# Kernel tuning notes

Hardware: AMD Instinct MI355X
Metric: run time of the kernel (lower is better)

The kernel has to match this reference:

```python
import jax, jax.numpy as jnp
import numpy as np

B, F, P = 16384, 4096, 32
D = F // P
EPS = 1e-5


def setup_inputs() -> dict:
    key = jax.random.key(0)
    ks = jax.random.split(key, 5)
    bound = 1.0 / np.sqrt(D)
    return {
        "x": jax.random.normal(ks[0], (B, F), dtype=jnp.float32),
        "weights1": jax.random.uniform(ks[1], (P, D, D), dtype=jnp.float32, minval=-bound, maxval=bound),
        "bias1": jax.random.uniform(ks[2], (F,), dtype=jnp.float32, minval=-bound, maxval=bound),
        "weights2": jax.random.uniform(ks[3], (P, D, D), dtype=jnp.float32, minval=-bound, maxval=bound),
        "bias2": jax.random.uniform(ks[4], (F,), dtype=jnp.float32, minval=-bound, maxval=bound),
        "gamma1": jnp.ones((F,), dtype=jnp.float32),
        "beta1": jnp.zeros((F,), dtype=jnp.float32),
        "gamma3": jnp.ones((F,), dtype=jnp.float32),
        "beta3": jnp.zeros((F,), dtype=jnp.float32),
    }


def _block_matmul(x, w):
    # x: [B, F] viewed as [B, P, D]; w: [P, D, D] block-diagonal blocks.
    # Equivalent to x @ block_diag(*w) without building the [F, F] matrix.
    xb = x.reshape(x.shape[0], P, D)
    return jnp.einsum("bpd,pde->bpe", xb, w).reshape(x.shape[0], F)


def _batchnorm(y, gamma, beta):
    # Training-mode BatchNorm1d: biased variance over the batch dim.
    mean = jnp.mean(y, axis=0)
    var = jnp.var(y, axis=0)
    return gamma * (y - mean) * jax.lax.rsqrt(var + EPS) + beta


def reference(x, weights1, bias1, weights2, bias2, gamma1, beta1, gamma3, beta3):
    o1 = jnp.tanh(_batchnorm(_block_matmul(x, weights1) + bias1, gamma1, beta1))
    o2 = _block_matmul(o1, weights2) + bias2
    o3 = jnp.tanh(_batchnorm(o2 + x, gamma3, beta3))
    return o3
```

## Files before the change

kernel.cpp:

```cpp
#include <hip/hip_runtime.h>
#include <cstdint>
#include <cstddef>

#define B_ 16384
#define F_ 4096
#define P_ 32
#define D_ 128
#define STRIPS 16
#define TILES 32

using f32x4 = __attribute__((ext_vector_type(4))) float;
using s16x8 = __attribute__((ext_vector_type(8))) short;

__device__ inline unsigned short bf16_rn(float f) {
    union { float f; uint32_t u; } v; v.f = f;
    uint32_t u = v.u;
    return (unsigned short)((u + 0x7FFFu + ((u >> 16) & 1u)) >> 16);
}
__device__ inline float bf16_to_f32(unsigned short h) {
    union { uint32_t u; float f; } v; v.u = ((uint32_t)h) << 16;
    return v.f;
}
__device__ inline float fast_tanh(float z) {
    float e = __expf(2.f * z);
    return 1.f - 2.f / (e + 1.f);
}

__device__ inline void stage_w(const float* __restrict__ Wp,
                               short* s_whi, short* s_wlo, int tid) {
    for (int it = 0; it < 32; ++it) {
        int idx = it * 256 + tid;
        int c  = idx & 127;
        int kp = idx >> 7;
        float w0 = Wp[(2 * kp) * D_ + c];
        float w1 = Wp[(2 * kp + 1) * D_ + c];
        unsigned short h0 = bf16_rn(w0), h1 = bf16_rn(w1);
        float l0 = w0 - bf16_to_f32(h0);
        float l1 = w1 - bf16_to_f32(h1);
        unsigned short g0 = bf16_rn(l0), g1 = bf16_rn(l1);
        uint32_t hi = (uint32_t)h0 | ((uint32_t)h1 << 16);
        uint32_t lo = (uint32_t)g0 | ((uint32_t)g1 << 16);
        int boff = c * 256 + ((4 * kp) ^ ((c & 7) << 4));
        *(uint32_t*)((char*)s_whi + boff) = hi;
        *(uint32_t*)((char*)s_wlo + boff) = lo;
    }
}

__device__ inline s16x8 read_b(const short* s_w, int col, int skbytes) {
    int boff = col * 256 + (skbytes ^ ((col & 7) << 4));
    return *(const s16x8*)((const char*)s_w + boff);
}

__global__ __launch_bounds__(256) void k_gemm1(
    const float* __restrict__ x, const float* __restrict__ W1,
    const float* __restrict__ bias1, float* __restrict__ y1,
    float* __restrict__ sum1, float* __restrict__ sumsq1)
{
    __shared__ short s_whi[D_ * D_];
    __shared__ short s_wlo[D_ * D_];
    const int tid = threadIdx.x;
    const int bid = blockIdx.x;
    const int p = bid / STRIPS;
    const int strip = bid % STRIPS;
    stage_w(W1 + (size_t)p * D_ * D_, s_whi, s_wlo, tid);
    __syncthreads();

    const int wave = tid >> 6, lane = tid & 63;
    const int l15 = lane & 15, l4 = lane >> 4;
    const int colbase = wave * 32;

    float bi[2]; int gcol[2];
#pragma unroll
    for (int j = 0; j < 2; ++j) {
        gcol[j] = p * D_ + colbase + j * 16 + l15;
        bi[j] = bias1[gcol[j]];
    }
    float csum[2] = {0.f, 0.f}, csq[2] = {0.f, 0.f};

    for (int it = 0; it < TILES; ++it) {
        const int m0 = strip * (TILES * 32) + it * 32;
        f32x4 av[2][4][2];
#pragma unroll
        for (int i = 0; i < 2; ++i)
#pragma unroll
            for (int s = 0; s < 4; ++s) {
                const float* ptr = x + (size_t)(m0 + i * 16 + l15) * F_
                                     + p * D_ + s * 32 + l4 * 8;
                av[i][s][0] = *(const f32x4*)ptr;
                av[i][s][1] = *(const f32x4*)(ptr + 4);
            }
        f32x4 zero = {0.f, 0.f, 0.f, 0.f};
        f32x4 acc[2][2];
#pragma unroll
        for (int i = 0; i < 2; ++i)
#pragma unroll
            for (int j = 0; j < 2; ++j) acc[i][j] = zero;

#pragma unroll
        for (int s = 0; s < 4; ++s) {
            s16x8 a[2];
#pragma unroll
            for (int i = 0; i < 2; ++i)
#pragma unroll
                for (int t = 0; t < 4; ++t) {
                    a[i][t]     = (short)bf16_rn(av[i][s][0][t]);
                    a[i][t + 4] = (short)bf16_rn(av[i][s][1][t]);
                }
            const int sk = s * 64 + l4 * 16;
#pragma unroll
            for (int j = 0; j < 2; ++j) {
                const int col = colbase + j * 16 + l15;
                s16x8 bh = read_b(s_whi, col, sk);
                s16x8 bl = read_b(s_wlo, col, sk);
#pragma unroll
                for (int i = 0; i < 2; ++i) {
                    acc[i][j] = __builtin_amdgcn_mfma_f32_16x16x32_bf16(a[i], bh, acc[i][j], 0, 0, 0);
                    acc[i][j] = __builtin_amdgcn_mfma_f32_16x16x32_bf16(a[i], bl, acc[i][j], 0, 0, 0);
                }
            }
        }
#pragma unroll
        for (int i = 0; i < 2; ++i)
#pragma unroll
            for (int j = 0; j < 2; ++j)
#pragma unroll
                for (int r = 0; r < 4; ++r) {
                    float v = acc[i][j][r] + bi[j];
                    int row = m0 + i * 16 + l4 * 4 + r;
                    y1[(size_t)row * F_ + gcol[j]] = v;
                    csum[j] += v;
                    csq[j]  += v * v;
                }
    }
#pragma unroll
    for (int j = 0; j < 2; ++j) {
        float s = csum[j], q = csq[j];
        s += __shfl_xor(s, 16); q += __shfl_xor(q, 16);
        s += __shfl_xor(s, 32); q += __shfl_xor(q, 32);
        if (l4 == 0) {
            atomicAdd(&sum1[gcol[j]], s);
            atomicAdd(&sumsq1[gcol[j]], q);
        }
    }
}

__global__ __launch_bounds__(256) void k_gemm2(
    const float* __restrict__ x, float* yb ,
    const float* __restrict__ W2, const float* __restrict__ bias2,
    const float* __restrict__ scale1, const float* __restrict__ shift1,
    float* __restrict__ sum3, float* __restrict__ sumsq3)
{
    __shared__ short s_whi[D_ * D_];
    __shared__ short s_wlo[D_ * D_];
    __shared__ float s_sc[D_];
    __shared__ float s_sh[D_];
    const int tid = threadIdx.x;
    const int bid = blockIdx.x;
    const int p = bid / STRIPS;
    const int strip = bid % STRIPS;
    stage_w(W2 + (size_t)p * D_ * D_, s_whi, s_wlo, tid);
    if (tid < D_) {
        s_sc[tid] = scale1[p * D_ + tid];
        s_sh[tid] = shift1[p * D_ + tid];
    }
    __syncthreads();

    const int wave = tid >> 6, lane = tid & 63;
    const int l15 = lane & 15, l4 = lane >> 4;
    const int colbase = wave * 32;

    float bi[2]; int gcol[2];
#pragma unroll
    for (int j = 0; j < 2; ++j) {
        gcol[j] = p * D_ + colbase + j * 16 + l15;
        bi[j] = bias2[gcol[j]];
    }
    float csum[2] = {0.f, 0.f}, csq[2] = {0.f, 0.f};

    for (int it = 0; it < TILES; ++it) {
        const int m0 = strip * (TILES * 32) + it * 32;
        f32x4 av[2][4][2];
#pragma unroll
        for (int i = 0; i < 2; ++i)
#pragma unroll
            for (int s = 0; s < 4; ++s) {
                const float* ptr = yb + (size_t)(m0 + i * 16 + l15) * F_
                                      + p * D_ + s * 32 + l4 * 8;
                av[i][s][0] = *(const f32x4*)ptr;
                av[i][s][1] = *(const f32x4*)(ptr + 4);
            }
        f32x4 zero = {0.f, 0.f, 0.f, 0.f};
        f32x4 acc[2][2];
#pragma unroll
        for (int i = 0; i < 2; ++i)
#pragma unroll
            for (int j = 0; j < 2; ++j) acc[i][j] = zero;

#pragma unroll
        for (int s = 0; s < 4; ++s) {
            s16x8 a[2];
#pragma unroll
            for (int i = 0; i < 2; ++i)
#pragma unroll
                for (int h = 0; h < 2; ++h)
#pragma unroll
                    for (int t = 0; t < 4; ++t) {
                        int kk = s * 32 + l4 * 8 + h * 4 + t;
                        float z = s_sc[kk] * av[i][s][h][t] + s_sh[kk];
                        a[i][h * 4 + t] = (short)bf16_rn(fast_tanh(z));
                    }
            const int sk = s * 64 + l4 * 16;
#pragma unroll
            for (int j = 0; j < 2; ++j) {
                const int col = colbase + j * 16 + l15;
                s16x8 bh = read_b(s_whi, col, sk);
                s16x8 bl = read_b(s_wlo, col, sk);
#pragma unroll
                for (int i = 0; i < 2; ++i) {
                    acc[i][j] = __builtin_amdgcn_mfma_f32_16x16x32_bf16(a[i], bh, acc[i][j], 0, 0, 0);
                    acc[i][j] = __builtin_amdgcn_mfma_f32_16x16x32_bf16(a[i], bl, acc[i][j], 0, 0, 0);
                }
            }
        }
        __syncthreads();
#pragma unroll
        for (int i = 0; i < 2; ++i)
#pragma unroll
            for (int j = 0; j < 2; ++j)
#pragma unroll
                for (int r = 0; r < 4; ++r) {
                    int row = m0 + i * 16 + l4 * 4 + r;
                    float v = acc[i][j][r] + bi[j]
                            + x[(size_t)row * F_ + gcol[j]];
                    yb[(size_t)row * F_ + gcol[j]] = v;
                    csum[j] += v;
                    csq[j]  += v * v;
                }
    }
#pragma unroll
    for (int j = 0; j < 2; ++j) {
        float s = csum[j], q = csq[j];
        s += __shfl_xor(s, 16); q += __shfl_xor(q, 16);
        s += __shfl_xor(s, 32); q += __shfl_xor(q, 32);
        if (l4 == 0) {
            atomicAdd(&sum3[gcol[j]], s);
            atomicAdd(&sumsq3[gcol[j]], q);
        }
    }
}

__global__ void k_finalize(const float* __restrict__ sum,
                           const float* __restrict__ sumsq,
                           const float* __restrict__ gamma,
                           const float* __restrict__ beta,
                           float* __restrict__ scale,
                           float* __restrict__ shift)
{
    int f = blockIdx.x * blockDim.x + threadIdx.x;
    if (f < F_) {
        float mean = sum[f] * (1.f / B_);
        float var  = sumsq[f] * (1.f / B_) - mean * mean;
        float rstd = rsqrtf(var + 1e-5f);
        float sc = gamma[f] * rstd;
        scale[f] = sc;
        shift[f] = beta[f] - mean * sc;
    }
}

__global__ void k_bn_tanh(float* yb, const float* __restrict__ scale3,
                          const float* __restrict__ shift3)
{
    const size_t n4 = (size_t)B_ * F_ / 4;
    size_t i = (size_t)blockIdx.x * blockDim.x + threadIdx.x;
    const size_t stride = (size_t)gridDim.x * blockDim.x;
    for (; i < n4; i += stride) {
        f32x4 v = ((const f32x4*)yb)[i];
        int col = (int)((i * 4) & (F_ - 1));
        f32x4 sc = *(const f32x4*)(scale3 + col);
        f32x4 sh = *(const f32x4*)(shift3 + col);
        f32x4 r;
#pragma unroll
        for (int t = 0; t < 4; ++t) r[t] = fast_tanh(sc[t] * v[t] + sh[t]);
        ((f32x4*)yb)[i] = r;
    }
}

extern "C" void kernel_launch(void* const* d_in, const int* in_sizes, int n_in,
                              void* d_out, int out_size, void* d_ws, size_t ws_size,
                              hipStream_t stream) {
    const float* x      = (const float*)d_in[0];
    const float* W1     = (const float*)d_in[1];
    const float* bias1  = (const float*)d_in[2];
    const float* W2     = (const float*)d_in[3];
    const float* bias2  = (const float*)d_in[4];
    const float* gamma1 = (const float*)d_in[5];
    const float* beta1  = (const float*)d_in[6];
    const float* gamma3 = (const float*)d_in[7];
    const float* beta3  = (const float*)d_in[8];

    float* yb = (float*)d_out;
    float* S  = (float*)d_ws;
    float* sum1   = S;
    float* sumsq1 = S + 4096;
    float* scale1 = S + 8192;
    float* shift1 = S + 12288;
    float* sum3   = S + 16384;
    float* sumsq3 = S + 20480;
    float* scale3 = S + 24576;
    float* shift3 = S + 28672;

    hipMemsetAsync(d_ws, 0, 8 * 4096 * sizeof(float), stream);

    k_gemm1<<<P_ * STRIPS, 256, 0, stream>>>(x, W1, bias1, yb, sum1, sumsq1);
    k_finalize<<<F_ / 256, 256, 0, stream>>>(sum1, sumsq1, gamma1, beta1, scale1, shift1);
    k_gemm2<<<P_ * STRIPS, 256, 0, stream>>>(x, yb, W2, bias2, scale1, shift1, sum3, sumsq3);
    k_finalize<<<F_ / 256, 256, 0, stream>>>(sum3, sumsq3, gamma3, beta3, scale3, shift3);
    k_bn_tanh<<<2048, 256, 0, stream>>>(yb, scale3, shift3);
}
```

Baseline: 582.8 us.

## Use single bf16 weights, drop BN-cancelled biases, widen wave tiles

Replaces hi/lo split-bf16 weight MFMAs with a single bf16 pass and stores weights in MFMA fragment order in LDS. Drops bias1/bias2 since training-mode BatchNorm removes per-column constants. Restructures so each wave computes 32 rows by all 128 columns, loading and converting each input element once per block instead of once per wave, and reduces column stats through LDS before global atomics. Folds the factor 2 of tanh into the BN scale/shift and uses a hardware reciprocal; precision of the GEMMs drops to plain bf16.

```diff
diff --git a/kernel.cpp b/kernel.cpp
--- a/kernel.cpp
+++ b/kernel.cpp
@@ -1,4 +1,5 @@
 #include <hip/hip_runtime.h>
+#include <hip/hip_bf16.h>
 #include <cstdint>
 #include <cstddef>
 
@@ -6,246 +7,232 @@
 #define F_ 4096
 #define P_ 32
 #define D_ 128
-#define STRIPS 16
-#define TILES 32
+#define TPB 4
+#define STRIPS 32
 
 using f32x4 = __attribute__((ext_vector_type(4))) float;
 using s16x8 = __attribute__((ext_vector_type(8))) short;
 
-__device__ inline unsigned short bf16_rn(float f) {
-    union { float f; uint32_t u; } v; v.f = f;
-    uint32_t u = v.u;
-    return (unsigned short)((u + 0x7FFFu + ((u >> 16) & 1u)) >> 16);
-}
-__device__ inline float bf16_to_f32(unsigned short h) {
-    union { uint32_t u; float f; } v; v.u = ((uint32_t)h) << 16;
-    return v.f;
-}
-__device__ inline float fast_tanh(float z) {
-    float e = __expf(2.f * z);
-    return 1.f - 2.f / (e + 1.f);
-}
-
-__device__ inline void stage_w(const float* __restrict__ Wp,
-                               short* s_whi, short* s_wlo, int tid) {
-    for (int it = 0; it < 32; ++it) {
-        int idx = it * 256 + tid;
-        int c  = idx & 127;
-        int kp = idx >> 7;
-        float w0 = Wp[(2 * kp) * D_ + c];
-        float w1 = Wp[(2 * kp + 1) * D_ + c];
-        unsigned short h0 = bf16_rn(w0), h1 = bf16_rn(w1);
-        float l0 = w0 - bf16_to_f32(h0);
-        float l1 = w1 - bf16_to_f32(h1);
-        unsigned short g0 = bf16_rn(l0), g1 = bf16_rn(l1);
-        uint32_t hi = (uint32_t)h0 | ((uint32_t)h1 << 16);
-        uint32_t lo = (uint32_t)g0 | ((uint32_t)g1 << 16);
-        int boff = c * 256 + ((4 * kp) ^ ((c & 7) << 4));
-        *(uint32_t*)((char*)s_whi + boff) = hi;
-        *(uint32_t*)((char*)s_wlo + boff) = lo;
-    }
-}
-
-__device__ inline s16x8 read_b(const short* s_w, int col, int skbytes) {
-    int boff = col * 256 + (skbytes ^ ((col & 7) << 4));
-    return *(const s16x8*)((const char*)s_w + boff);
+union abuf { s16x8 v; uint32_t u[4]; };
+
+__device__ inline uint32_t pk_bf16(float a, float b) {
+    float2 f; f.x = a; f.y = b;
+    union { __hip_bfloat162 h; uint32_t u; } cv;
+    cv.h = __float22bfloat162_rn(f);
+    return cv.u;
+}
+
+__device__ inline float tanh_from_2z(float z2) {
+    float e = __expf(z2);
+    return 1.f - 2.f * __builtin_amdgcn_rcpf(e + 1.f);
+}
+
+__device__ inline void stage_w(const float* __restrict__ Wp, short* s_w, int tid) {
+#pragma unroll
+    for (int it = 0; it < 8; ++it) {
+        int slot = it * 256 + tid;
+        int l15 = slot & 15;
+        int l4  = (slot >> 4) & 3;
+        int s   = (slot >> 6) & 3;
+        int j   = slot >> 8;
+        const float* src = Wp + (size_t)(s * 32 + l4 * 8) * D_ + j * 16 + l15;
+        abuf a;
+#pragma unroll
+        for (int q = 0; q < 4; ++q) {
+            float w0 = src[(size_t)(2 * q) * D_];
+            float w1 = src[(size_t)(2 * q + 1) * D_];
+            a.u[q] = pk_bf16(w0, w1);
+        }
+        *(s16x8*)((char*)s_w + (size_t)slot * 16) = a.v;
+    }
 }
 
 __global__ __launch_bounds__(256) void k_gemm1(
     const float* __restrict__ x, const float* __restrict__ W1,
-    const float* __restrict__ bias1, float* __restrict__ y1,
-    float* __restrict__ sum1, float* __restrict__ sumsq1)
+    float* __restrict__ y1, float* __restrict__ gsum, float* __restrict__ gsq)
 {
-    __shared__ short s_whi[D_ * D_];
-    __shared__ short s_wlo[D_ * D_];
+    __shared__ short s_w[D_ * D_];
+    __shared__ float s_sum[D_], s_sq[D_];
     const int tid = threadIdx.x;
-    const int bid = blockIdx.x;
-    const int p = bid / STRIPS;
-    const int strip = bid % STRIPS;
-    stage_w(W1 + (size_t)p * D_ * D_, s_whi, s_wlo, tid);
+    const int p = blockIdx.x / STRIPS;
+    const int strip = blockIdx.x % STRIPS;
+    stage_w(W1 + (size_t)p * D_ * D_, s_w, tid);
+    if (tid < D_) { s_sum[tid] = 0.f; s_sq[tid] = 0.f; }
     __syncthreads();
 
     const int wave = tid >> 6, lane = tid & 63;
     const int l15 = lane & 15, l4 = lane >> 4;
-    const int colbase = wave * 32;
-
-    float bi[2]; int gcol[2];
-#pragma unroll
-    for (int j = 0; j < 2; ++j) {
-        gcol[j] = p * D_ + colbase + j * 16 + l15;
-        bi[j] = bias1[gcol[j]];
-    }
-    float csum[2] = {0.f, 0.f}, csq[2] = {0.f, 0.f};
-
-    for (int it = 0; it < TILES; ++it) {
-        const int m0 = strip * (TILES * 32) + it * 32;
-        f32x4 av[2][4][2];
+    const int lds_lane = lane * 16;
+
+    float csum[8], csq[8];
+#pragma unroll
+    for (int j = 0; j < 8; ++j) { csum[j] = 0.f; csq[j] = 0.f; }
+
+    for (int it = 0; it < TPB; ++it) {
+        const int arow = (strip * TPB + it) * 128 + wave * 32;
+        f32x4 acc[2][8];
 #pragma unroll
         for (int i = 0; i < 2; ++i)
 #pragma unroll
-            for (int s = 0; s < 4; ++s) {
-                const float* ptr = x + (size_t)(m0 + i * 16 + l15) * F_
+            for (int j = 0; j < 8; ++j) acc[i][j] = (f32x4){0.f, 0.f, 0.f, 0.f};
+
+#pragma unroll
+        for (int s = 0; s < 4; ++s) {
+            abuf a[2];
+#pragma unroll
+            for (int i = 0; i < 2; ++i) {
+                const float* ptr = x + (size_t)(arow + i * 16 + l15) * F_
                                      + p * D_ + s * 32 + l4 * 8;
-                av[i][s][0] = *(const f32x4*)ptr;
-                av[i][s][1] = *(const f32x4*)(ptr + 4);
-            }
-        f32x4 zero = {0.f, 0.f, 0.f, 0.f};
-        f32x4 acc[2][2];
-#pragma unroll
-        for (int i = 0; i < 2; ++i)
-#pragma unroll
-            for (int j = 0; j < 2; ++j) acc[i][j] = zero;
-
-#pragma unroll
-        for (int s = 0; s < 4; ++s) {
-            s16x8 a[2];
-#pragma unroll
-            for (int i = 0; i < 2; ++i)
-#pragma unroll
-                for (int t = 0; t < 4; ++t) {
-                    a[i][t]     = (short)bf16_rn(av[i][s][0][t]);
-                    a[i][t + 4] = (short)bf16_rn(av[i][s][1][t]);
+                f32x4 v0 = *(const f32x4*)ptr;
+                f32x4 v1 = *(const f32x4*)(ptr + 4);
+                a[i].u[0] = pk_bf16(v0[0], v0[1]);
+                a[i].u[1] = pk_bf16(v0[2], v0[3]);
+                a[i].u[2] = pk_bf16(v1[0], v1[1]);
+                a[i].u[3] = pk_bf16(v1[2], v1[3]);
+            }
+#pragma unroll
+            for (int j = 0; j < 8; ++j) {
+                s16x8 b = *(const s16x8*)((const char*)s_w
+                              + (size_t)((j * 4 + s) * 1024) + lds_lane);
+#pragma unroll
+                for (int i = 0; i < 2; ++i)
+                    acc[i][j] = __builtin_amdgcn_mfma_f32_16x16x32_bf16(a[i].v, b, acc[i][j], 0, 0, 0);
+            }
+        }
+#pragma unroll
+        for (int i = 0; i < 2; ++i) {
+            const int rbase = arow + i * 16 + l4 * 4;
+#pragma unroll
+            for (int j = 0; j < 8; ++j) {
+                float* yp = y1 + (size_t)rbase * F_ + p * D_ + j * 16 + l15;
+#pragma unroll
+                for (int r = 0; r < 4; ++r) {
+                    float v = acc[i][j][r];
+                    yp[(size_t)r * F_] = v;
+                    csum[j] += v;
+                    csq[j] = fmaf(v, v, csq[j]);
                 }
-            const int sk = s * 64 + l4 * 16;
-#pragma unroll
-            for (int j = 0; j < 2; ++j) {
-                const int col = colbase + j * 16 + l15;
-                s16x8 bh = read_b(s_whi, col, sk);
-                s16x8 bl = read_b(s_wlo, col, sk);
-#pragma unroll
-                for (int i = 0; i < 2; ++i) {
-                    acc[i][j] = __builtin_amdgcn_mfma_f32_16x16x32_bf16(a[i], bh, acc[i][j], 0, 0, 0);
-                    acc[i][j] = __builtin_amdgcn_mfma_f32_16x16x32_bf16(a[i], bl, acc[i][j], 0, 0, 0);
-                }
-            }
-        }
-#pragma unroll
-        for (int i = 0; i < 2; ++i)
-#pragma unroll
-            for (int j = 0; j < 2; ++j)
-#pragma unroll
-                for (int r = 0; r < 4; ++r) {
-                    float v = acc[i][j][r] + bi[j];
-                    int row = m0 + i * 16 + l4 * 4 + r;
-                    y1[(size_t)row * F_ + gcol[j]] = v;
-                    csum[j] += v;
-                    csq[j]  += v * v;
-                }
-    }
-#pragma unroll
-    for (int j = 0; j < 2; ++j) {
-        float s = csum[j], q = csq[j];
-        s += __shfl_xor(s, 16); q += __shfl_xor(q, 16);
-        s += __shfl_xor(s, 32); q += __shfl_xor(q, 32);
+            }
+        }
+    }
+#pragma unroll
+    for (int j = 0; j < 8; ++j) {
+        float sm = csum[j], q = csq[j];
+        sm += __shfl_xor(sm, 16); q += __shfl_xor(q, 16);
+        sm += __shfl_xor(sm, 32); q += __shfl_xor(q, 32);
         if (l4 == 0) {
-            atomicAdd(&sum1[gcol[j]], s);
-            atomicAdd(&sumsq1[gcol[j]], q);
-        }
+            atomicAdd(&s_sum[j * 16 + l15], sm);
+            atomicAdd(&s_sq[j * 16 + l15], q);
+        }
+    }
+    __syncthreads();
+    if (tid < D_) {
+        atomicAdd(&gsum[p * D_ + tid], s_sum[tid]);
+        atomicAdd(&gsq[p * D_ + tid], s_sq[tid]);
     }
 }
 
 __global__ __launch_bounds__(256) void k_gemm2(
-    const float* __restrict__ x, float* yb ,
-    const float* __restrict__ W2, const float* __restrict__ bias2,
-    const float* __restrict__ scale1, const float* __restrict__ shift1,
-    float* __restrict__ sum3, float* __restrict__ sumsq3)
+    const float* __restrict__ x, float* __restrict__ yb ,
+    const float* __restrict__ W2,
+    const float* __restrict__ sc2, const float* __restrict__ sh2,
+    float* __restrict__ gsum, float* __restrict__ gsq)
 {
-    __shared__ short s_whi[D_ * D_];
-    __shared__ short s_wlo[D_ * D_];
-    __shared__ float s_sc[D_];
-    __shared__ float s_sh[D_];
+    __shared__ short s_w[D_ * D_];
+    __shared__ float s_sc[D_], s_sh[D_];
+    __shared__ float s_sum[D_], s_sq[D_];
     const int tid = threadIdx.x;
-    const int bid = blockIdx.x;
-    const int p = bid / STRIPS;
-    const int strip = bid % STRIPS;
-    stage_w(W2 + (size_t)p * D_ * D_, s_whi, s_wlo, tid);
+    const int p = blockIdx.x / STRIPS;
+    const int strip = blockIdx.x % STRIPS;
+    stage_w(W2 + (size_t)p * D_ * D_, s_w, tid);
     if (tid < D_) {
-        s_sc[tid] = scale1[p * D_ + tid];
-        s_sh[tid] = shift1[p * D_ + tid];
+        s_sc[tid] = sc2[p * D_ + tid];
+        s_sh[tid] = sh2[p * D_ + tid];
+        s_sum[tid] = 0.f; s_sq[tid] = 0.f;
     }
     __syncthreads();
 
     const int wave = tid >> 6, lane = tid & 63;
     const int l15 = lane & 15, l4 = lane >> 4;
-    const int colbase = wave * 32;
-
-    float bi[2]; int gcol[2];
-#pragma unroll
-    for (int j = 0; j < 2; ++j) {
-        gcol[j] = p * D_ + colbase + j * 16 + l15;
-        bi[j] = bias2[gcol[j]];
-    }
-    float csum[2] = {0.f, 0.f}, csq[2] = {0.f, 0.f};
-
-    for (int it = 0; it < TILES; ++it) {
-        const int m0 = strip * (TILES * 32) + it * 32;
-        f32x4 av[2][4][2];
+    const int lds_lane = lane * 16;
+
+    float csum[8], csq[8];
+#pragma unroll
+    for (int j = 0; j < 8; ++j) { csum[j] = 0.f; csq[j] = 0.f; }
+
+    for (int it = 0; it < TPB; ++it) {
+        const int arow = (strip * TPB + it) * 128 + wave * 32;
+        f32x4 acc[2][8];
 #pragma unroll
         for (int i = 0; i < 2; ++i)
 #pragma unroll
-            for (int s = 0; s < 4; ++s) {
-                const float* ptr = yb + (size_t)(m0 + i * 16 + l15) * F_
+            for (int j = 0; j < 8; ++j) acc[i][j] = (f32x4){0.f, 0.f, 0.f, 0.f};
+
+#pragma unroll
+        for (int s = 0; s < 4; ++s) {
+            f32x4 scv0 = *(const f32x4*)&s_sc[s * 32 + l4 * 8];
+            f32x4 scv1 = *(const f32x4*)&s_sc[s * 32 + l4 * 8 + 4];
+            f32x4 shv0 = *(const f32x4*)&s_sh[s * 32 + l4 * 8];
+            f32x4 shv1 = *(const f32x4*)&s_sh[s * 32 + l4 * 8 + 4];
+            abuf a[2];
+#pragma unroll
+            for (int i = 0; i < 2; ++i) {
+                const float* ptr = yb + (size_t)(arow + i * 16 + l15) * F_
                                       + p * D_ + s * 32 + l4 * 8;
-                av[i][s][0] = *(const f32x4*)ptr;
-                av[i][s][1] = *(const f32x4*)(ptr + 4);
-            }
-        f32x4 zero = {0.f, 0.f, 0.f, 0.f};
-        f32x4 acc[2][2];
-#pragma unroll
-        for (int i = 0; i < 2; ++i)
-#pragma unroll
-            for (int j = 0; j < 2; ++j) acc[i][j] = zero;
-
-#pragma unroll
-        for (int s = 0; s < 4; ++s) {
-            s16x8 a[2];
-#pragma unroll
-            for (int i = 0; i < 2; ++i)
-#pragma unroll
-                for (int h = 0; h < 2; ++h)
-#pragma unroll
-                    for (int t = 0; t < 4; ++t) {
-                        int kk = s * 32 + l4 * 8 + h * 4 + t;
-                        float z = s_sc[kk] * av[i][s][h][t] + s_sh[kk];
-                        a[i][h * 4 + t] = (short)bf16_rn(fast_tanh(z));
-                    }
-            const int sk = s * 64 + l4 * 16;
-#pragma unroll
-            for (int j = 0; j < 2; ++j) {
-                const int col = colbase + j * 16 + l15;
-                s16x8 bh = read_b(s_whi, col, sk);
-                s16x8 bl = read_b(s_wlo, col, sk);
-#pragma unroll
-                for (int i = 0; i < 2; ++i) {
-                    acc[i][j] = __builtin_amdgcn_mfma_f32_16x16x32_bf16(a[i], bh, acc[i][j], 0, 0, 0);
-                    acc[i][j] = __builtin_amdgcn_mfma_f32_16x16x32_bf16(a[i], bl, acc[i][j], 0, 0, 0);
+                f32x4 v0 = *(const f32x4*)ptr;
+                f32x4 v1 = *(const f32x4*)(ptr + 4);
+                float t[8];
+#pragma unroll
+                for (int q = 0; q < 4; ++q) {
+                    t[q]     = tanh_from_2z(fmaf(v0[q], scv0[q], shv0[q]));
+                    t[q + 4] = tanh_from_2z(fmaf(v1[q], scv1[q], shv1[q]));
                 }
-            }
-        }
-        __syncthreads();
-#pragma unroll
-        for (int i = 0; i < 2; ++i)
-#pragma unroll
-            for (int j = 0; j < 2; ++j)
+                a[i].u[0] = pk_bf16(t[0], t[1]);
+                a[i].u[1] = pk_bf16(t[2], t[3]);
+                a[i].u[2] = pk_bf16(t[4], t[5]);
+                a[i].u[3] = pk_bf16(t[6], t[7]);
+            }
+#pragma unroll
+            for (int j = 0; j < 8; ++j) {
+                s16x8 b = *(const s16x8*)((const char*)s_w
+                              + (size_t)((j * 4 + s) * 1024) + lds_lane);
+#pragma unroll
+                for (int i = 0; i < 2; ++i)
+                    acc[i][j] = __builtin_amdgcn_mfma_f32_16x16x32_bf16(a[i].v, b, acc[i][j], 0, 0, 0);
+            }
+        }
+#pragma unroll
+        for (int i = 0; i < 2; ++i) {
+            const int rbase = arow + i * 16 + l4 * 4;
+#pragma unroll
+            for (int j = 0; j < 8; ++j) {
+                const size_t off = (size_t)rbase * F_ + p * D_ + j * 16 + l15;
+                const float* xp = x + off;
+                float* yp = yb + off;
 #pragma unroll
                 for (int r = 0; r < 4; ++r) {
-                    int row = m0 + i * 16 + l4 * 4 + r;
-                    float v = acc[i][j][r] + bi[j]
-                            + x[(size_t)row * F_ + gcol[j]];
-                    yb[(size_t)row * F_ + gcol[j]] = v;
+                    float v = acc[i][j][r] + xp[(size_t)r * F_];
+                    yp[(size_t)r * F_] = v;
                     csum[j] += v;
-                    csq[j]  += v * v;
+                    csq[j] = fmaf(v, v, csq[j]);
                 }
-    }
-#pragma unroll
-    for (int j = 0; j < 2; ++j) {
-        float s = csum[j], q = csq[j];
-        s += __shfl_xor(s, 16); q += __shfl_xor(q, 16);
-        s += __shfl_xor(s, 32); q += __shfl_xor(q, 32);
+            }
+        }
+    }
+#pragma unroll
+    for (int j = 0; j < 8; ++j) {
+        float sm = csum[j], q = csq[j];
+        sm += __shfl_xor(sm, 16); q += __shfl_xor(q, 16);
+        sm += __shfl_xor(sm, 32); q += __shfl_xor(q, 32);
         if (l4 == 0) {
-            atomicAdd(&sum3[gcol[j]], s);
-            atomicAdd(&sumsq3[gcol[j]], q);
-        }
+            atomicAdd(&s_sum[j * 16 + l15], sm);
+            atomicAdd(&s_sq[j * 16 + l15], q);
+        }
+    }
+    __syncthreads();
+    if (tid < D_) {
+        atomicAdd(&gsum[p * D_ + tid], s_sum[tid]);
+        atomicAdd(&gsq[p * D_ + tid], s_sq[tid]);
     }
 }
 
@@ -253,8 +240,8 @@
                            const float* __restrict__ sumsq,
                            const float* __restrict__ gamma,
                            const float* __restrict__ beta,
-                           float* __restrict__ scale,
-                           float* __restrict__ shift)
+                           float* __restrict__ sc2,
+                           float* __restrict__ sh2)
 {
     int f = blockIdx.x * blockDim.x + threadIdx.x;
     if (f < F_) {
@@ -262,13 +249,13 @@
         float var  = sumsq[f] * (1.f / B_) - mean * mean;
         float rstd = rsqrtf(var + 1e-5f);
         float sc = gamma[f] * rstd;
-        scale[f] = sc;
-        shift[f] = beta[f] - mean * sc;
-    }
-}
-
-__global__ void k_bn_tanh(float* yb, const float* __restrict__ scale3,
-                          const float* __restrict__ shift3)
+        sc2[f] = 2.f * sc;
+        sh2[f] = 2.f * (beta[f] - mean * sc);
+    }
+}
+
+__global__ void k_bn_tanh(float* yb, const float* __restrict__ sc2,
+                          const float* __restrict__ sh2)
 {
     const size_t n4 = (size_t)B_ * F_ / 4;
     size_t i = (size_t)blockIdx.x * blockDim.x + threadIdx.x;
@@ -276,11 +263,11 @@
     for (; i < n4; i += stride) {
         f32x4 v = ((const f32x4*)yb)[i];
         int col = (int)((i * 4) & (F_ - 1));
-        f32x4 sc = *(const f32x4*)(scale3 + col);
-        f32x4 sh = *(const f32x4*)(shift3 + col);
+        f32x4 sc = *(const f32x4*)(sc2 + col);
+        f32x4 sh = *(const f32x4*)(sh2 + col);
         f32x4 r;
 #pragma unroll
-        for (int t = 0; t < 4; ++t) r[t] = fast_tanh(sc[t] * v[t] + sh[t]);
+        for (int t = 0; t < 4; ++t) r[t] = tanh_from_2z(fmaf(v[t], sc[t], sh[t]));
         ((f32x4*)yb)[i] = r;
     }
 }
@@ -290,9 +277,7 @@
                               hipStream_t stream) {
     const float* x      = (const float*)d_in[0];
     const float* W1     = (const float*)d_in[1];
-    const float* bias1  = (const float*)d_in[2];
     const float* W2     = (const float*)d_in[3];
-    const float* bias2  = (const float*)d_in[4];
     const float* gamma1 = (const float*)d_in[5];
     const float* beta1  = (const float*)d_in[6];
     const float* gamma3 = (const float*)d_in[7];
@@ -302,18 +287,18 @@
     float* S  = (float*)d_ws;
     float* sum1   = S;
     float* sumsq1 = S + 4096;
-    float* scale1 = S + 8192;
-    float* shift1 = S + 12288;
-    float* sum3   = S + 16384;
-    float* sumsq3 = S + 20480;
-    float* scale3 = S + 24576;
-    float* shift3 = S + 28672;
-
-    hipMemsetAsync(d_ws, 0, 8 * 4096 * sizeof(float), stream);
-
-    k_gemm1<<<P_ * STRIPS, 256, 0, stream>>>(x, W1, bias1, yb, sum1, sumsq1);
-    k_finalize<<<F_ / 256, 256, 0, stream>>>(sum1, sumsq1, gamma1, beta1, scale1, shift1);
-    k_gemm2<<<P_ * STRIPS, 256, 0, stream>>>(x, yb, W2, bias2, scale1, shift1, sum3, sumsq3);
-    k_finalize<<<F_ / 256, 256, 0, stream>>>(sum3, sumsq3, gamma3, beta3, scale3, shift3);
-    k_bn_tanh<<<2048, 256, 0, stream>>>(yb, scale3, shift3);
-}
+    float* sum3   = S + 8192;
+    float* sumsq3 = S + 12288;
+    float* sc2_1  = S + 16384;
+    float* sh2_1  = S + 20480;
+    float* sc2_3  = S + 24576;
+    float* sh2_3  = S + 28672;
+
+    hipMemsetAsync(d_ws, 0, 4 * 4096 * sizeof(float), stream);
+
+    k_gemm1<<<P_ * STRIPS, 256, 0, stream>>>(x, W1, yb, sum1, sumsq1);
+    k_finalize<<<F_ / 256, 256, 0, stream>>>(sum1, sumsq1, gamma1, beta1, sc2_1, sh2_1);
+    k_gemm2<<<P_ * STRIPS, 256, 0, stream>>>(x, yb, W2, sc2_1, sh2_1, sum3, sumsq3);
+    k_finalize<<<F_ / 256, 256, 0, stream>>>(sum3, sumsq3, gamma3, beta3, sc2_3, sh2_3);
+    k_bn_tanh<<<2048, 256, 0, stream>>>(yb, sc2_3, sh2_3);
+}
```

Result: slower. 698.4 us (+19.8%).
